# Kernel optimization log

Measured on AMD Instinct MI355X. Metric: run time of the kernel, lower is better.

## Reference

```python
import jax, jax.numpy as jnp
import numpy as np


def _unfold(x, k):
    # x: [B, C, H, W] -> [B, C, S, L] with S=k*k (row-major patch order), L=H*W
    B, C, H, W = x.shape
    pad = k // 2
    xp = jnp.pad(x, ((0, 0), (0, 0), (pad, pad), (pad, pad)))
    patches = jnp.stack(
        [xp[:, :, r:r + H, c:c + W] for r in range(k) for c in range(k)], axis=2
    )  # [B, C, S, H, W]
    return patches.reshape(B, C, k * k, H * W)


def setup_inputs() -> dict:
    key = jax.random.key(0)
    ks = jax.random.split(key, 8)
    B, C, H, W = 8, 64, 128, 128
    R, Cout = 4, 128
    x = jax.random.normal(ks[0], (B, C, H, W), dtype=jnp.float32)
    gate_w = jax.random.normal(ks[1], (R, C), dtype=jnp.float32) * 0.05   # 1x1 gate conv weight
    gate_b = jax.random.normal(ks[2], (R,), dtype=jnp.float32) * 0.01
    theta = jax.random.normal(ks[3], (R,), dtype=jnp.float32) * 0.5       # learned directions
    raw_sigma_u = jax.random.normal(ks[4], (R,), dtype=jnp.float32) * 0.1
    raw_sigma_s = jax.random.normal(ks[5], (R,), dtype=jnp.float32) * 0.1
    pw_w = jax.random.normal(ks[6], (Cout, R * C), dtype=jnp.float32) * (1.0 / np.sqrt(R * C).astype(np.float32))
    pw_b = jax.random.normal(ks[7], (Cout,), dtype=jnp.float32) * 0.01
    return {"x": x, "gate_w": gate_w, "gate_b": gate_b, "theta": theta,
            "raw_sigma_u": raw_sigma_u, "raw_sigma_s": raw_sigma_s,
            "pw_w": pw_w, "pw_b": pw_b}


def reference(x, gate_w, gate_b, theta, raw_sigma_u, raw_sigma_s, pw_w, pw_b):
    k = 3
    B, C, H, W = x.shape
    R = theta.shape[0]
    S, L = k * k, H * W

    x_un = _unfold(x, k)                                         # [B, C, S, L]

    # 1x1 gate conv + fuzzy softmax over rules
    logits = jnp.einsum('bchw,rc->brhw', x, gate_w) + gate_b[None, :, None, None]
    mu = jax.nn.softmax(logits, axis=1)                          # [B, R, H, W]
    mu_un = _unfold(mu, k)                                       # [B, R, S, L]
    s_center = (k // 2) * k + (k // 2)
    mu_center = mu_un[:, :, s_center:s_center + 1, :]            # [B, R, 1, L]

    # anisotropic Gaussian kernel per rule over integer offsets (row-major)
    grid = np.arange(k, dtype=np.float32) - k // 2
    dy = jnp.asarray(np.repeat(grid, k))                         # [S]
    dx = jnp.asarray(np.tile(grid, k))                           # [S]
    cos_t, sin_t = jnp.cos(theta)[:, None], jnp.sin(theta)[:, None]
    proj_u = cos_t * dx[None, :] + sin_t * dy[None, :]           # [R, S]
    proj_s = -sin_t * dx[None, :] + cos_t * dy[None, :]
    su = (jax.nn.softplus(raw_sigma_u) + 1e-4)[:, None]
    ss = (jax.nn.softplus(raw_sigma_s) + 1e-4)[:, None]
    kern = jnp.exp(-proj_u ** 2 / su ** 2 - proj_s ** 2 / ss ** 2)  # [R, S]

    alpha = mu_center * mu_un * kern[None, :, :, None]           # [B, R, S, L]
    alpha_sum = jnp.maximum(alpha.sum(axis=(1, 2), keepdims=True), 1e-8)
    alpha = alpha / alpha_sum

    agg = jnp.einsum('brsl,bcsl->brcl', alpha, x_un)             # [B, R, C, L]
    agg_flat = agg.reshape(B, R * C, L)
    out = jnp.einsum('bnl,on->bol', agg_flat, pw_w) + pw_b[None, :, None]
    return out.reshape(B, -1, H, W)
```

## Files before the change

### kernel.cpp

```cpp
#include <hip/hip_runtime.h>
#include <math.h>

#define CC 64
#define RR 4
#define HH 128
#define WW 128
#define BB 8
#define COUT 128
#define XCH 164

typedef __attribute__((ext_vector_type(8))) short short8;
typedef __attribute__((ext_vector_type(4))) float f32x4;
typedef __attribute__((ext_vector_type(2))) float f32x2;

__device__ __forceinline__ unsigned short f2bf(float f) {
  unsigned u = __float_as_uint(f);
  u += 0x7fffu + ((u >> 16) & 1u);
  return (unsigned short)(u >> 16);
}
__device__ __forceinline__ float bf2f(unsigned short h) {
  return __uint_as_float(((unsigned)h) << 16);
}

__global__ __launch_bounds__(256) void k_pre(const float* __restrict__ theta,
                                             const float* __restrict__ rsu,
                                             const float* __restrict__ rss,
                                             const float* __restrict__ pw,
                                             float* __restrict__ wkern,
                                             unsigned short* __restrict__ pwb) {
  int i = blockIdx.x * 256 + threadIdx.x;
  if (i < COUT * RR * CC) pwb[i] = f2bf(pw[i]);
  if (blockIdx.x == 0 && threadIdx.x < RR * 9) {
    int t = threadIdx.x;
    int r = t / 9, s = t % 9;
    float dy = (float)(s / 3 - 1), dx = (float)(s % 3 - 1);
    float ct = cosf(theta[r]), st = sinf(theta[r]);
    float su = log1pf(expf(rsu[r])) + 1e-4f;
    float sv = log1pf(expf(rss[r])) + 1e-4f;
    float pu = ct * dx + st * dy;
    float ps = -st * dx + ct * dy;
    wkern[t] = expf(-(pu * pu) / (su * su) - (ps * ps) / (sv * sv));
  }
}

__global__ __launch_bounds__(256, 3) void k_fused(const float* __restrict__ x,
                                                  const float* __restrict__ gw,
                                                  const float* __restrict__ gb,
                                                  const float* __restrict__ wkern,
                                                  const unsigned short* __restrict__ pwb,
                                                  const float* __restrict__ pb,
                                                  float* __restrict__ out) {
  __shared__ unsigned short xs[CC][XCH];
  __shared__ float mus[RR][4][40];
  __shared__ float alp[36][64];
  __shared__ float rsum[RR][64];
  __shared__ unsigned short aggs[32][264];

  int tid = threadIdx.x;
  int raw = blockIdx.x;
  int bid = (raw & 7) * 256 + (raw >> 3);
  int b = bid >> 8;
  int rem = bid & 255;
  int h0 = (rem >> 2) << 1;
  int w0 = (rem & 3) << 5;

  {
    int c4 = tid & 15;
    int pr0 = tid >> 4;
    if (c4 < 10) {
      int gcol = w0 - 4 + (c4 << 2);
      bool colok = (unsigned)gcol < WW;
      #pragma unroll
      for (int k = 0; k < 16; ++k) {
        int pair = (k << 4) + pr0;
        int c = pair >> 2, row = pair & 3;
        int grow = h0 - 1 + row;
        float4 v = make_float4(0.f, 0.f, 0.f, 0.f);
        if (colok && (unsigned)grow < HH)
          v = *(const float4*)(x + (((size_t)b * CC + c) << 14) + (grow << 7) + gcol);
        ushort4 uv;
        uv.x = f2bf(v.x); uv.y = f2bf(v.y); uv.z = f2bf(v.z); uv.w = f2bf(v.w);
        *(ushort4*)&xs[c][row * 40 + (c4 << 2)] = uv;
      }
    }
  }
  __syncthreads();

  if (tid < 136) {
    int y = tid / 34, cxo = tid % 34;
    int cx = 3 + cxo;
    int grow = h0 - 1 + y, gcol = w0 - 1 + cxo;
    float lg0 = gb[0], lg1 = gb[1], lg2 = gb[2], lg3 = gb[3];
    #pragma unroll 8
    for (int c = 0; c < CC; ++c) {
      float xv = bf2f(xs[c][y * 40 + cx]);
      lg0 = fmaf(xv, gw[c], lg0);
      lg1 = fmaf(xv, gw[64 + c], lg1);
      lg2 = fmaf(xv, gw[128 + c], lg2);
      lg3 = fmaf(xv, gw[192 + c], lg3);
    }
    float m = fmaxf(fmaxf(lg0, lg1), fmaxf(lg2, lg3));
    float e0 = expf(lg0 - m), e1 = expf(lg1 - m);
    float e2 = expf(lg2 - m), e3 = expf(lg3 - m);
    float inv = 1.0f / (e0 + e1 + e2 + e3);
    if (!((unsigned)grow < HH && (unsigned)gcol < WW)) inv = 0.0f;
    mus[0][y][cx] = e0 * inv;
    mus[1][y][cx] = e1 * inv;
    mus[2][y][cx] = e2 * inv;
    mus[3][y][cx] = e3 * inv;
  }
  __syncthreads();

  {
    int t = tid & 63, r = tid >> 6;
    int prow = t >> 5, pcol = t & 31;
    float mc = mus[r][prow + 1][pcol + 4];
    float sum = 0.f;
    #pragma unroll
    for (int s = 0; s < 9; ++s) {
      int sr = s / 3, sc = s % 3;
      float a = mc * mus[r][prow + sr][pcol + 3 + sc] * wkern[r * 9 + s];
      alp[r * 9 + s][t] = a;
      sum += a;
    }
    rsum[r][t] = sum;
  }

  int lane = tid & 63;
  int wv = tid >> 6;
  int lr = lane & 15, lq = lane >> 4;
  int o0 = wv << 5;

  short8 a0r[8], a1r[8];
  {
    const unsigned short* pA = pwb + ((o0 + lr) << 8) + (lq << 3);
    #pragma unroll
    for (int ks = 0; ks < 8; ++ks) {
      a0r[ks] = *(const short8*)(pA + (ks << 5));
      a1r[ks] = *(const short8*)(pA + 4096 + (ks << 5));
    }
  }
  __syncthreads();

  #pragma unroll
  for (int p = 0; p < 2; ++p) {
    {
      int t = tid & 31, cg = tid >> 5, c0 = cg << 3;
      int px = (p << 5) + t;
      float inv = 1.0f / fmaxf(rsum[0][px] + rsum[1][px] + rsum[2][px] + rsum[3][px], 1e-8f);
      f32x2 cacc[4][4];
      #pragma unroll
      for (int r = 0; r < 4; ++r)
        #pragma unroll
        for (int j = 0; j < 4; ++j) cacc[r][j] = (f32x2){0.f, 0.f};

      #pragma unroll
      for (int s = 0; s < 9; ++s) {
        int sr = s / 3, sc = s % 3;
        int xo = (p + sr) * 40 + t + 3 + sc;
        f32x2 xv[4];
        #pragma unroll
        for (int j = 0; j < 4; ++j) {
          xv[j][0] = bf2f(xs[c0 + 2 * j][xo]);
          xv[j][1] = bf2f(xs[c0 + 2 * j + 1][xo]);
        }
        #pragma unroll
        for (int r = 0; r < 4; ++r) {
          float av = alp[r * 9 + s][px];
          f32x2 av2 = {av, av};
          #pragma unroll
          for (int j = 0; j < 4; ++j) cacc[r][j] += av2 * xv[j];
        }
      }
      #pragma unroll
      for (int r = 0; r < 4; ++r) {
        short8 wvv;
        #pragma unroll
        for (int j = 0; j < 4; ++j) {
          wvv[2 * j]     = (short)f2bf(cacc[r][j][0] * inv);
          wvv[2 * j + 1] = (short)f2bf(cacc[r][j][1] * inv);
        }
        *(short8*)&aggs[t][(r << 6) + c0] = wvv;
      }
    }
    __syncthreads();

    f32x4 dacc[2][2];
    #pragma unroll
    for (int i = 0; i < 2; ++i)
      #pragma unroll
      for (int j = 0; j < 2; ++j) dacc[i][j] = (f32x4){0.f, 0.f, 0.f, 0.f};

    #pragma unroll
    for (int ks = 0; ks < 8; ++ks) {
      short8 b0 = *(const short8*)&aggs[lr][(ks << 5) + (lq << 3)];
      short8 b1 = *(const short8*)&aggs[16 + lr][(ks << 5) + (lq << 3)];
      dacc[0][0] = __builtin_amdgcn_mfma_f32_16x16x32_bf16(a0r[ks], b0, dacc[0][0], 0, 0, 0);
      dacc[0][1] = __builtin_amdgcn_mfma_f32_16x16x32_bf16(a0r[ks], b1, dacc[0][1], 0, 0, 0);
      dacc[1][0] = __builtin_amdgcn_mfma_f32_16x16x32_bf16(a1r[ks], b0, dacc[1][0], 0, 0, 0);
      dacc[1][1] = __builtin_amdgcn_mfma_f32_16x16x32_bf16(a1r[ks], b1, dacc[1][1], 0, 0, 0);
    }

    #pragma unroll
    for (int oi = 0; oi < 2; ++oi) {
      #pragma unroll
      for (int q = 0; q < 4; ++q) {
        int o = o0 + (oi << 4) + (lq << 2) + q;
        float bias = pb[o];
        size_t base = (((size_t)b * COUT + o) << 14) + ((h0 + p) << 7) + w0;
        out[base + lr]      = dacc[oi][0][q] + bias;
        out[base + 16 + lr] = dacc[oi][1][q] + bias;
      }
    }
    if (p == 0) __syncthreads();
  }
}

extern "C" void kernel_launch(void* const* d_in, const int* in_sizes, int n_in,
                              void* d_out, int out_size, void* d_ws, size_t ws_size,
                              hipStream_t stream) {
  const float* x     = (const float*)d_in[0];
  const float* gw    = (const float*)d_in[1];
  const float* gb    = (const float*)d_in[2];
  const float* theta = (const float*)d_in[3];
  const float* rsu   = (const float*)d_in[4];
  const float* rss   = (const float*)d_in[5];
  const float* pw    = (const float*)d_in[6];
  const float* pb    = (const float*)d_in[7];
  float* outp = (float*)d_out;

  float* wkern = (float*)d_ws;
  unsigned short* pwb = (unsigned short*)(wkern + 64);

  k_pre<<<128, 256, 0, stream>>>(theta, rsu, rss, pw, wkern, pwb);
  k_fused<<<BB * (HH / 2) * (WW / 32), 256, 0, stream>>>(x, gw, gb, wkern, pwb, pb, outp);
}
```

Measured before the change: 60.27 us.

## Shrink LDS footprint, store normalized bf16 alphas, process 16-pixel rounds for higher occupancy

The kernel now computes the Gaussian kernel weights inside the fused kernel rather than in k_pre. Alphas are normalized before aggregation and stored as bf16 in a pixel-major layout, and rsum is aliased into the aggs buffer. The aggregation/MFMA stage runs in four rounds of 16 pixels with a smaller aggs tile, and the x tile load is reorganized to use all threads. Together these cut LDS usage and raise launch_bounds to 4 blocks per CU, aiming to improve latency hiding. In exchange there are extra syncs and rounds, plus bf16 rounding of the alphas.

```diff
diff --git a/kernel.cpp b/kernel.cpp
--- a/kernel.cpp
+++ b/kernel.cpp
@@ -22,39 +22,26 @@
   return __uint_as_float(((unsigned)h) << 16);
 }
 
-__global__ __launch_bounds__(256) void k_pre(const float* __restrict__ theta,
-                                             const float* __restrict__ rsu,
-                                             const float* __restrict__ rss,
-                                             const float* __restrict__ pw,
-                                             float* __restrict__ wkern,
+__global__ __launch_bounds__(256) void k_pre(const float* __restrict__ pw,
                                              unsigned short* __restrict__ pwb) {
   int i = blockIdx.x * 256 + threadIdx.x;
-  if (i < COUT * RR * CC) pwb[i] = f2bf(pw[i]);
-  if (blockIdx.x == 0 && threadIdx.x < RR * 9) {
-    int t = threadIdx.x;
-    int r = t / 9, s = t % 9;
-    float dy = (float)(s / 3 - 1), dx = (float)(s % 3 - 1);
-    float ct = cosf(theta[r]), st = sinf(theta[r]);
-    float su = log1pf(expf(rsu[r])) + 1e-4f;
-    float sv = log1pf(expf(rss[r])) + 1e-4f;
-    float pu = ct * dx + st * dy;
-    float ps = -st * dx + ct * dy;
-    wkern[t] = expf(-(pu * pu) / (su * su) - (ps * ps) / (sv * sv));
-  }
-}
-
-__global__ __launch_bounds__(256, 3) void k_fused(const float* __restrict__ x,
+  pwb[i] = f2bf(pw[i]);
+}
+
+__global__ __launch_bounds__(256, 4) void k_fused(const float* __restrict__ x,
                                                   const float* __restrict__ gw,
                                                   const float* __restrict__ gb,
-                                                  const float* __restrict__ wkern,
+                                                  const float* __restrict__ theta,
+                                                  const float* __restrict__ rsu,
+                                                  const float* __restrict__ rss,
                                                   const unsigned short* __restrict__ pwb,
                                                   const float* __restrict__ pb,
                                                   float* __restrict__ out) {
   __shared__ unsigned short xs[CC][XCH];
   __shared__ float mus[RR][4][40];
-  __shared__ float alp[36][64];
-  __shared__ float rsum[RR][64];
-  __shared__ unsigned short aggs[32][264];
+  __shared__ unsigned short alp[64][40];
+  __shared__ __align__(16) unsigned short aggs[16][264];
+  float* rsum = (float*)&aggs[0][0];
 
   int tid = threadIdx.x;
   int raw = blockIdx.x;
@@ -64,25 +51,48 @@
   int h0 = (rem >> 2) << 1;
   int w0 = (rem & 3) << 5;
 
+  int lane = tid & 63;
+  int wv = tid >> 6;
+  int lr = lane & 15, lq = lane >> 4;
+  int o0 = wv << 5;
+
+  short8 a0r[8], a1r[8];
   {
-    int c4 = tid & 15;
-    int pr0 = tid >> 4;
-    if (c4 < 10) {
-      int gcol = w0 - 4 + (c4 << 2);
-      bool colok = (unsigned)gcol < WW;
-      #pragma unroll
-      for (int k = 0; k < 16; ++k) {
-        int pair = (k << 4) + pr0;
-        int c = pair >> 2, row = pair & 3;
-        int grow = h0 - 1 + row;
-        float4 v = make_float4(0.f, 0.f, 0.f, 0.f);
-        if (colok && (unsigned)grow < HH)
-          v = *(const float4*)(x + (((size_t)b * CC + c) << 14) + (grow << 7) + gcol);
-        ushort4 uv;
-        uv.x = f2bf(v.x); uv.y = f2bf(v.y); uv.z = f2bf(v.z); uv.w = f2bf(v.w);
-        *(ushort4*)&xs[c][row * 40 + (c4 << 2)] = uv;
-      }
-    }
+    const unsigned short* pA = pwb + ((o0 + lr) << 8) + (lq << 3);
+    #pragma unroll
+    for (int ks = 0; ks < 8; ++ks) {
+      a0r[ks] = *(const short8*)(pA + (ks << 5));
+      a1r[ks] = *(const short8*)(pA + 4096 + (ks << 5));
+    }
+  }
+  float4 pbv0 = *(const float4*)&pb[o0 + (lq << 2)];
+  float4 pbv1 = *(const float4*)&pb[o0 + 16 + (lq << 2)];
+
+  #pragma unroll
+  for (int k = 0; k < 8; ++k) {
+    int i = (k << 8) + tid;
+    int c4 = i & 7, c = (i >> 3) & 63, row = (i >> 9) & 3;
+    int gcol = w0 - 4 + (c4 << 2);
+    int grow = h0 - 1 + row;
+    float4 v = make_float4(0.f, 0.f, 0.f, 0.f);
+    if ((unsigned)gcol < WW && (unsigned)grow < HH)
+      v = *(const float4*)(x + (((size_t)b * CC + c) << 14) + (grow << 7) + gcol);
+    ushort4 uv;
+    uv.x = f2bf(v.x); uv.y = f2bf(v.y); uv.z = f2bf(v.z); uv.w = f2bf(v.w);
+    *(ushort4*)&xs[c][row * 40 + (c4 << 2)] = uv;
+  }
+  #pragma unroll
+  for (int k = 0; k < 2; ++k) {
+    int i = (k << 8) + tid;
+    int slot = i & 1, c = (i >> 1) & 63, row = (i >> 7) & 3;
+    int gcol = w0 - 4 + 32 + (slot << 2);
+    int grow = h0 - 1 + row;
+    float4 v = make_float4(0.f, 0.f, 0.f, 0.f);
+    if ((unsigned)gcol < WW && (unsigned)grow < HH)
+      v = *(const float4*)(x + (((size_t)b * CC + c) << 14) + (grow << 7) + gcol);
+    ushort4 uv;
+    uv.x = f2bf(v.x); uv.y = f2bf(v.y); uv.z = f2bf(v.z); uv.w = f2bf(v.w);
+    *(ushort4*)&xs[c][row * 40 + 32 + (slot << 2)] = uv;
   }
   __syncthreads();
 
@@ -111,108 +121,100 @@
   }
   __syncthreads();
 
+  float a9[9];
   {
     int t = tid & 63, r = tid >> 6;
+    float th = theta[r];
+    float ct = cosf(th), st = sinf(th);
+    float su = log1pf(expf(rsu[r])) + 1e-4f;
+    float sv = log1pf(expf(rss[r])) + 1e-4f;
+    float isu = 1.0f / (su * su), isv = 1.0f / (sv * sv);
     int prow = t >> 5, pcol = t & 31;
     float mc = mus[r][prow + 1][pcol + 4];
     float sum = 0.f;
     #pragma unroll
     for (int s = 0; s < 9; ++s) {
-      int sr = s / 3, sc = s % 3;
-      float a = mc * mus[r][prow + sr][pcol + 3 + sc] * wkern[r * 9 + s];
-      alp[r * 9 + s][t] = a;
-      sum += a;
-    }
-    rsum[r][t] = sum;
-  }
-
-  int lane = tid & 63;
-  int wv = tid >> 6;
-  int lr = lane & 15, lq = lane >> 4;
-  int o0 = wv << 5;
-
-  short8 a0r[8], a1r[8];
+      float dy = (float)(s / 3 - 1), dx = (float)(s % 3 - 1);
+      float pu = ct * dx + st * dy;
+      float ps = -st * dx + ct * dy;
+      float kern = expf(-pu * pu * isu - ps * ps * isv);
+      float av = mc * mus[r][prow + s / 3][pcol + 3 + s % 3] * kern;
+      a9[s] = av;
+      sum += av;
+    }
+    rsum[(r << 6) + t] = sum;
+  }
+  __syncthreads();
+
   {
-    const unsigned short* pA = pwb + ((o0 + lr) << 8) + (lq << 3);
+    int t = tid & 63, r = tid >> 6;
+    float tot = rsum[t] + rsum[64 + t] + rsum[128 + t] + rsum[192 + t];
+    float inv = 1.0f / fmaxf(tot, 1e-8f);
     #pragma unroll
-    for (int ks = 0; ks < 8; ++ks) {
-      a0r[ks] = *(const short8*)(pA + (ks << 5));
-      a1r[ks] = *(const short8*)(pA + 4096 + (ks << 5));
-    }
+    for (int s = 0; s < 9; ++s)
+      alp[t][(s << 2) + r] = f2bf(a9[s] * inv);
   }
   __syncthreads();
 
   #pragma unroll
-  for (int p = 0; p < 2; ++p) {
+  for (int rd = 0; rd < 4; ++rd) {
     {
-      int t = tid & 31, cg = tid >> 5, c0 = cg << 3;
-      int px = (p << 5) + t;
-      float inv = 1.0f / fmaxf(rsum[0][px] + rsum[1][px] + rsum[2][px] + rsum[3][px], 1e-8f);
-      f32x2 cacc[4][4];
-      #pragma unroll
-      for (int r = 0; r < 4; ++r)
-        #pragma unroll
-        for (int j = 0; j < 4; ++j) cacc[r][j] = (f32x2){0.f, 0.f};
-
+      int t16 = tid & 15, cg = tid >> 4, c0 = cg << 2;
+      int px = (rd << 4) + t16;
+      int prow2 = px >> 5, pc = px & 31;
+      f32x2 cacc[4][2];
+      #pragma unroll
+      for (int r = 0; r < 4; ++r) {
+        cacc[r][0] = (f32x2){0.f, 0.f};
+        cacc[r][1] = (f32x2){0.f, 0.f};
+      }
+      const unsigned short* arow = &alp[px][0];
       #pragma unroll
       for (int s = 0; s < 9; ++s) {
-        int sr = s / 3, sc = s % 3;
-        int xo = (p + sr) * 40 + t + 3 + sc;
-        f32x2 xv[4];
-        #pragma unroll
-        for (int j = 0; j < 4; ++j) {
-          xv[j][0] = bf2f(xs[c0 + 2 * j][xo]);
-          xv[j][1] = bf2f(xs[c0 + 2 * j + 1][xo]);
-        }
-        #pragma unroll
-        for (int r = 0; r < 4; ++r) {
-          float av = alp[r * 9 + s][px];
-          f32x2 av2 = {av, av};
-          #pragma unroll
-          for (int j = 0; j < 4; ++j) cacc[r][j] += av2 * xv[j];
-        }
+        uint2 ad = *(const uint2*)(arow + (s << 2));
+        float af0 = __uint_as_float(ad.x << 16);
+        float af1 = __uint_as_float(ad.x & 0xffff0000u);
+        float af2 = __uint_as_float(ad.y << 16);
+        float af3 = __uint_as_float(ad.y & 0xffff0000u);
+        int xo = (prow2 + s / 3) * 40 + pc + 3 + s % 3;
+        f32x2 xv0, xv1;
+        xv0[0] = bf2f(xs[c0][xo]);     xv0[1] = bf2f(xs[c0 + 1][xo]);
+        xv1[0] = bf2f(xs[c0 + 2][xo]); xv1[1] = bf2f(xs[c0 + 3][xo]);
+        f32x2 A0 = {af0, af0}, A1 = {af1, af1}, A2 = {af2, af2}, A3 = {af3, af3};
+        cacc[0][0] += A0 * xv0; cacc[0][1] += A0 * xv1;
+        cacc[1][0] += A1 * xv0; cacc[1][1] += A1 * xv1;
+        cacc[2][0] += A2 * xv0; cacc[2][1] += A2 * xv1;
+        cacc[3][0] += A3 * xv0; cacc[3][1] += A3 * xv1;
       }
       #pragma unroll
       for (int r = 0; r < 4; ++r) {
-        short8 wvv;
-        #pragma unroll
-        for (int j = 0; j < 4; ++j) {
-          wvv[2 * j]     = (short)f2bf(cacc[r][j][0] * inv);
-          wvv[2 * j + 1] = (short)f2bf(cacc[r][j][1] * inv);
-        }
-        *(short8*)&aggs[t][(r << 6) + c0] = wvv;
+        ushort4 wvv;
+        wvv.x = f2bf(cacc[r][0][0]); wvv.y = f2bf(cacc[r][0][1]);
+        wvv.z = f2bf(cacc[r][1][0]); wvv.w = f2bf(cacc[r][1][1]);
+        *(ushort4*)&aggs[t16][(r << 6) + c0] = wvv;
       }
     }
     __syncthreads();
 
-    f32x4 dacc[2][2];
-    #pragma unroll
-    for (int i = 0; i < 2; ++i)
-      #pragma unroll
-      for (int j = 0; j < 2; ++j) dacc[i][j] = (f32x4){0.f, 0.f, 0.f, 0.f};
-
-    #pragma unroll
-    for (int ks = 0; ks < 8; ++ks) {
-      short8 b0 = *(const short8*)&aggs[lr][(ks << 5) + (lq << 3)];
-      short8 b1 = *(const short8*)&aggs[16 + lr][(ks << 5) + (lq << 3)];
-      dacc[0][0] = __builtin_amdgcn_mfma_f32_16x16x32_bf16(a0r[ks], b0, dacc[0][0], 0, 0, 0);
-      dacc[0][1] = __builtin_amdgcn_mfma_f32_16x16x32_bf16(a0r[ks], b1, dacc[0][1], 0, 0, 0);
-      dacc[1][0] = __builtin_amdgcn_mfma_f32_16x16x32_bf16(a1r[ks], b0, dacc[1][0], 0, 0, 0);
-      dacc[1][1] = __builtin_amdgcn_mfma_f32_16x16x32_bf16(a1r[ks], b1, dacc[1][1], 0, 0, 0);
-    }
-
-    #pragma unroll
-    for (int oi = 0; oi < 2; ++oi) {
+    {
+      f32x4 dacc0 = (f32x4){0.f, 0.f, 0.f, 0.f};
+      f32x4 dacc1 = (f32x4){0.f, 0.f, 0.f, 0.f};
+      #pragma unroll
+      for (int ks = 0; ks < 8; ++ks) {
+        short8 b0 = *(const short8*)&aggs[lr][(ks << 5) + (lq << 3)];
+        dacc0 = __builtin_amdgcn_mfma_f32_16x16x32_bf16(a0r[ks], b0, dacc0, 0, 0, 0);
+        dacc1 = __builtin_amdgcn_mfma_f32_16x16x32_bf16(a1r[ks], b0, dacc1, 0, 0, 0);
+      }
+      int orow = h0 + (rd >> 1);
+      int oc = w0 + ((rd & 1) << 4) + lr;
       #pragma unroll
       for (int q = 0; q < 4; ++q) {
-        int o = o0 + (oi << 4) + (lq << 2) + q;
-        float bias = pb[o];
-        size_t base = (((size_t)b * COUT + o) << 14) + ((h0 + p) << 7) + w0;
-        out[base + lr]      = dacc[oi][0][q] + bias;
-        out[base + 16 + lr] = dacc[oi][1][q] + bias;
-      }
-    }
-    if (p == 0) __syncthreads();
+        int o = o0 + (lq << 2) + q;
+        out[(((size_t)b * COUT + o) << 14) + (orow << 7) + oc] = dacc0[q] + pbv0[q];
+        out[(((size_t)b * COUT + o + 16) << 14) + (orow << 7) + oc] = dacc1[q] + pbv1[q];
+      }
+    }
+    if (rd < 3) __syncthreads();
   }
 }
 
@@ -229,9 +231,9 @@
   const float* pb    = (const float*)d_in[7];
   float* outp = (float*)d_out;
 
-  float* wkern = (float*)d_ws;
-  unsigned short* pwb = (unsigned short*)(wkern + 64);
-
-  k_pre<<<128, 256, 0, stream>>>(theta, rsu, rss, pw, wkern, pwb);
-  k_fused<<<BB * (HH / 2) * (WW / 32), 256, 0, stream>>>(x, gw, gb, wkern, pwb, pb, outp);
-}
+  unsigned short* pwb = (unsigned short*)d_ws;
+
+  k_pre<<<(COUT * RR * CC) / 256, 256, 0, stream>>>(pw, pwb);
+  k_fused<<<BB * (HH / 2) * (WW / 32), 256, 0, stream>>>(x, gw, gb, theta, rsu, rss,
+                                                         pwb, pb, outp);
+}
```

Result: slower. 100.7 us (+67.1%).

## Restructure aggregation into 16-pixel rounds with bf16 packed alpha

Applied to the files above, without the earlier changes.

The aggregation/GEMM loop is split into four rounds of 16 pixels instead of two rounds of 32. Each thread now handles 4 channels rather than 8, and alpha is stored as bf16 packed per pixel so it can be read with vector loads. x loads are double-buffered across the 9 taps, the pw weight fragments and bias are loaded at kernel start, and output stores are buffered across pairs of rounds. The aggregation buffer is halved in size, which should help register and LDS pressure. The cost is more barriers and extra bf16 rounding of alpha.

```diff
diff --git a/kernel.cpp b/kernel.cpp
--- a/kernel.cpp
+++ b/kernel.cpp
@@ -8,6 +8,7 @@
 #define BB 8
 #define COUT 128
 #define XCH 164
+#define ALS 44
 
 typedef __attribute__((ext_vector_type(8))) short short8;
 typedef __attribute__((ext_vector_type(4))) float f32x4;
@@ -52,9 +53,9 @@
                                                   float* __restrict__ out) {
   __shared__ unsigned short xs[CC][XCH];
   __shared__ float mus[RR][4][40];
-  __shared__ float alp[36][64];
+  __shared__ unsigned short alp[64][ALS];
   __shared__ float rsum[RR][64];
-  __shared__ unsigned short aggs[32][264];
+  __shared__ __align__(16) unsigned short aggs[16][264];
 
   int tid = threadIdx.x;
   int raw = blockIdx.x;
@@ -63,6 +64,23 @@
   int rem = bid & 255;
   int h0 = (rem >> 2) << 1;
   int w0 = (rem & 3) << 5;
+
+  int lane = tid & 63;
+  int wv = tid >> 6;
+  int lr = lane & 15, lq = lane >> 4;
+  int o0 = wv << 5;
+
+  short8 a0r[8], a1r[8];
+  {
+    const unsigned short* pA = pwb + ((o0 + lr) << 8) + (lq << 3);
+    #pragma unroll
+    for (int ks = 0; ks < 8; ++ks) {
+      a0r[ks] = *(const short8*)(pA + (ks << 5));
+      a1r[ks] = *(const short8*)(pA + 4096 + (ks << 5));
+    }
+  }
+  float4 pbv0 = *(const float4*)&pb[o0 + (lq << 2)];
+  float4 pbv1 = *(const float4*)&pb[o0 + 16 + (lq << 2)];
 
   {
     int c4 = tid & 15;
@@ -118,101 +136,99 @@
     float sum = 0.f;
     #pragma unroll
     for (int s = 0; s < 9; ++s) {
-      int sr = s / 3, sc = s % 3;
-      float a = mc * mus[r][prow + sr][pcol + 3 + sc] * wkern[r * 9 + s];
-      alp[r * 9 + s][t] = a;
-      sum += a;
+      float av = mc * mus[r][prow + s / 3][pcol + 3 + s % 3] * wkern[r * 9 + s];
+      alp[t][(s << 2) + r] = f2bf(av);
+      sum += av;
     }
     rsum[r][t] = sum;
   }
-
-  int lane = tid & 63;
-  int wv = tid >> 6;
-  int lr = lane & 15, lq = lane >> 4;
-  int o0 = wv << 5;
-
-  short8 a0r[8], a1r[8];
-  {
-    const unsigned short* pA = pwb + ((o0 + lr) << 8) + (lq << 3);
-    #pragma unroll
-    for (int ks = 0; ks < 8; ++ks) {
-      a0r[ks] = *(const short8*)(pA + (ks << 5));
-      a1r[ks] = *(const short8*)(pA + 4096 + (ks << 5));
-    }
-  }
   __syncthreads();
 
+  f32x4 dprev0 = (f32x4){0.f, 0.f, 0.f, 0.f};
+  f32x4 dprev1 = (f32x4){0.f, 0.f, 0.f, 0.f};
   #pragma unroll
-  for (int p = 0; p < 2; ++p) {
+  for (int rd = 0; rd < 4; ++rd) {
     {
-      int t = tid & 31, cg = tid >> 5, c0 = cg << 3;
-      int px = (p << 5) + t;
+      int t16 = tid & 15, cg = tid >> 4, c0 = cg << 2;
+      int px = (rd << 4) + t16;
+      int prow2 = px >> 5, pc = px & 31;
       float inv = 1.0f / fmaxf(rsum[0][px] + rsum[1][px] + rsum[2][px] + rsum[3][px], 1e-8f);
-      f32x2 cacc[4][4];
-      #pragma unroll
-      for (int r = 0; r < 4; ++r)
+
+      uint2 ad[9];
+      #pragma unroll
+      for (int s = 0; s < 9; ++s) ad[s] = *(const uint2*)(&alp[px][s << 2]);
+
+      f32x2 cacc[4][2];
+      #pragma unroll
+      for (int r = 0; r < 4; ++r) {
+        cacc[r][0] = (f32x2){0.f, 0.f};
+        cacc[r][1] = (f32x2){0.f, 0.f};
+      }
+
+      f32x2 xv[2][2];
+      {
+        int xo = prow2 * 40 + pc + 3;
+        xv[0][0][0] = bf2f(xs[c0][xo]);     xv[0][0][1] = bf2f(xs[c0 + 1][xo]);
+        xv[0][1][0] = bf2f(xs[c0 + 2][xo]); xv[0][1][1] = bf2f(xs[c0 + 3][xo]);
+      }
+      #pragma unroll
+      for (int s = 0; s < 9; ++s) {
+        if (s < 8) {
+          int sn = s + 1;
+          int xo = (prow2 + sn / 3) * 40 + pc + 3 + sn % 3;
+          xv[(s + 1) & 1][0][0] = bf2f(xs[c0][xo]);
+          xv[(s + 1) & 1][0][1] = bf2f(xs[c0 + 1][xo]);
+          xv[(s + 1) & 1][1][0] = bf2f(xs[c0 + 2][xo]);
+          xv[(s + 1) & 1][1][1] = bf2f(xs[c0 + 3][xo]);
+        }
+        unsigned adx = ad[s].x, ady = ad[s].y;
+        float af0 = __uint_as_float(adx << 16);
+        float af1 = __uint_as_float(adx & 0xffff0000u);
+        float af2 = __uint_as_float(ady << 16);
+        float af3 = __uint_as_float(ady & 0xffff0000u);
+        f32x2 A0 = {af0, af0}, A1 = {af1, af1}, A2 = {af2, af2}, A3 = {af3, af3};
+        f32x2 x0 = xv[s & 1][0], x1 = xv[s & 1][1];
+        cacc[0][0] += A0 * x0; cacc[0][1] += A0 * x1;
+        cacc[1][0] += A1 * x0; cacc[1][1] += A1 * x1;
+        cacc[2][0] += A2 * x0; cacc[2][1] += A2 * x1;
+        cacc[3][0] += A3 * x0; cacc[3][1] += A3 * x1;
+      }
+      #pragma unroll
+      for (int r = 0; r < 4; ++r) {
+        ushort4 wvv;
+        wvv.x = f2bf(cacc[r][0][0] * inv); wvv.y = f2bf(cacc[r][0][1] * inv);
+        wvv.z = f2bf(cacc[r][1][0] * inv); wvv.w = f2bf(cacc[r][1][1] * inv);
+        *(ushort4*)&aggs[t16][(r << 6) + c0] = wvv;
+      }
+    }
+    __syncthreads();
+
+    {
+      f32x4 dacc0 = (f32x4){0.f, 0.f, 0.f, 0.f};
+      f32x4 dacc1 = (f32x4){0.f, 0.f, 0.f, 0.f};
+      #pragma unroll
+      for (int ks = 0; ks < 8; ++ks) {
+        short8 b0 = *(const short8*)&aggs[lr][(ks << 5) + (lq << 3)];
+        dacc0 = __builtin_amdgcn_mfma_f32_16x16x32_bf16(a0r[ks], b0, dacc0, 0, 0, 0);
+        dacc1 = __builtin_amdgcn_mfma_f32_16x16x32_bf16(a1r[ks], b0, dacc1, 0, 0, 0);
+      }
+      if ((rd & 1) == 0) {
+        dprev0 = dacc0; dprev1 = dacc1;
+      } else {
+        int orow = h0 + (rd >> 1);
         #pragma unroll
-        for (int j = 0; j < 4; ++j) cacc[r][j] = (f32x2){0.f, 0.f};
-
-      #pragma unroll
-      for (int s = 0; s < 9; ++s) {
-        int sr = s / 3, sc = s % 3;
-        int xo = (p + sr) * 40 + t + 3 + sc;
-        f32x2 xv[4];
-        #pragma unroll
-        for (int j = 0; j < 4; ++j) {
-          xv[j][0] = bf2f(xs[c0 + 2 * j][xo]);
-          xv[j][1] = bf2f(xs[c0 + 2 * j + 1][xo]);
+        for (int q = 0; q < 4; ++q) {
+          int o = o0 + (lq << 2) + q;
+          size_t base0 = (((size_t)b * COUT + o) << 14) + (orow << 7) + w0;
+          size_t base1 = (((size_t)b * COUT + o + 16) << 14) + (orow << 7) + w0;
+          out[base0 + lr]      = dprev0[q] + pbv0[q];
+          out[base0 + 16 + lr] = dacc0[q] + pbv0[q];
+          out[base1 + lr]      = dprev1[q] + pbv1[q];
+          out[base1 + 16 + lr] = dacc1[q] + pbv1[q];
         }
-        #pragma unroll
-        for (int r = 0; r < 4; ++r) {
-          float av = alp[r * 9 + s][px];
-          f32x2 av2 = {av, av};
-          #pragma unroll
-          for (int j = 0; j < 4; ++j) cacc[r][j] += av2 * xv[j];
-        }
-      }
-      #pragma unroll
-      for (int r = 0; r < 4; ++r) {
-        short8 wvv;
-        #pragma unroll
-        for (int j = 0; j < 4; ++j) {
-          wvv[2 * j]     = (short)f2bf(cacc[r][j][0] * inv);
-          wvv[2 * j + 1] = (short)f2bf(cacc[r][j][1] * inv);
-        }
-        *(short8*)&aggs[t][(r << 6) + c0] = wvv;
-      }
-    }
-    __syncthreads();
-
-    f32x4 dacc[2][2];
-    #pragma unroll
-    for (int i = 0; i < 2; ++i)
-      #pragma unroll
-      for (int j = 0; j < 2; ++j) dacc[i][j] = (f32x4){0.f, 0.f, 0.f, 0.f};
-
-    #pragma unroll
-    for (int ks = 0; ks < 8; ++ks) {
-      short8 b0 = *(const short8*)&aggs[lr][(ks << 5) + (lq << 3)];
-      short8 b1 = *(const short8*)&aggs[16 + lr][(ks << 5) + (lq << 3)];
-      dacc[0][0] = __builtin_amdgcn_mfma_f32_16x16x32_bf16(a0r[ks], b0, dacc[0][0], 0, 0, 0);
-      dacc[0][1] = __builtin_amdgcn_mfma_f32_16x16x32_bf16(a0r[ks], b1, dacc[0][1], 0, 0, 0);
-      dacc[1][0] = __builtin_amdgcn_mfma_f32_16x16x32_bf16(a1r[ks], b0, dacc[1][0], 0, 0, 0);
-      dacc[1][1] = __builtin_amdgcn_mfma_f32_16x16x32_bf16(a1r[ks], b1, dacc[1][1], 0, 0, 0);
-    }
-
-    #pragma unroll
-    for (int oi = 0; oi < 2; ++oi) {
-      #pragma unroll
-      for (int q = 0; q < 4; ++q) {
-        int o = o0 + (oi << 4) + (lq << 2) + q;
-        float bias = pb[o];
-        size_t base = (((size_t)b * COUT + o) << 14) + ((h0 + p) << 7) + w0;
-        out[base + lr]      = dacc[oi][0][q] + bias;
-        out[base + 16 + lr] = dacc[oi][1][q] + bias;
-      }
-    }
-    if (p == 0) __syncthreads();
+      }
+    }
+    if (rd < 3) __syncthreads();
   }
 }
 
```

New measurement: 66.09 us. 9.7% more time.
